# Kernel tuning notes

Measured on AMD Instinct MI355X. Metric: run time of the kernel, lower is better.

The kernel has to match this reference:

```python
import jax, jax.numpy as jnp
import numpy as np

H = 50  # hidden size hard-coded in the module

def _lstm_cell(x, h, c, Wih, Whh, bih, bhh):
    # torch.nn.LSTMCell: gates ordered i, f, g, o
    g = x @ Wih.T + bih + h @ Whh.T + bhh  # [B, 4H]
    i, f, gg, o = jnp.split(g, 4, axis=-1)
    c2 = jax.nn.sigmoid(f) * c + jax.nn.sigmoid(i) * jnp.tanh(gg)
    h2 = jax.nn.sigmoid(o) * jnp.tanh(c2)
    return h2, c2

def setup_inputs() -> dict:
    key = jax.random.key(0)
    ks = jax.random.split(key, 10)
    B, T = 2048, 1024
    s1 = 1.0 / np.sqrt(H)
    u = lambda k, shp: jax.random.uniform(k, shp, jnp.float32, -s1, s1)
    return {
        "x": jax.random.normal(ks[0], (B, T), jnp.float32),
        "W_ih1": u(ks[1], (4 * H, 1)),
        "W_hh1": u(ks[2], (4 * H, H)),
        "b_ih1": u(ks[3], (4 * H,)),
        "b_hh1": u(ks[4], (4 * H,)),
        "W_ih2": u(ks[5], (4 * H, H)),
        "W_hh2": u(ks[6], (4 * H, H)),
        "b_ih2": u(ks[7], (4 * H,)),
        "b_hh2": u(ks[8], (4 * H,)),
        "W_lin": u(ks[9], (1, H)),
        "b_lin": jnp.zeros((1,), jnp.float32),
    }

def reference(x, W_ih1, W_hh1, b_ih1, b_hh1, W_ih2, W_hh2, b_ih2, b_hh2, W_lin, b_lin):
    # future=0 path; dropout is identity in eval mode.
    B = x.shape[0]
    xT = x.T[:, :, None]  # [T, B, 1]
    z = jnp.zeros((B, H), x.dtype)

    def step(carry, xt):
        h1, c1, h2, c2 = carry
        h1, c1 = _lstm_cell(xt, h1, c1, W_ih1, W_hh1, b_ih1, b_hh1)
        h2, c2 = _lstm_cell(h1, h2, c2, W_ih2, W_hh2, b_ih2, b_hh2)
        return (h1, c1, h2, c2), None

    (h1, c1, h2, c2), _ = jax.lax.scan(step, (z, z, z, z), xT)
    # outputs[:, -1] == linear(h_t2) at the final timestep
    out = h2 @ W_lin.T + b_lin  # [B, 1]
    return out[:, 0]
```

## Files before the change

### kernel.cpp

```cpp
#include <hip/hip_runtime.h>


#define TT 1024
#define HH 50
#define NB 8
#define NT 832
#define NTILE 13
#define VSZ 2112

typedef _Float16 f16x8 __attribute__((ext_vector_type(8)));
typedef unsigned short ushort8 __attribute__((ext_vector_type(8)));
typedef float f32x4 __attribute__((ext_vector_type(4)));

#define NLOG2E  -1.4426950408889634f
#define N2LOG2E -2.8853900817779268f

__device__ __forceinline__ float fast_rcp(float x) { return __builtin_amdgcn_rcpf(x); }
__device__ __forceinline__ float exp2f_hw(float x) { return __builtin_amdgcn_exp2f(x); }
__device__ __forceinline__ unsigned short f16bits(float f) {
    _Float16 h = (_Float16)f;
    return __builtin_bit_cast(unsigned short, h);
}
__device__ __forceinline__ float f16tof(unsigned short b) {
    return (float)__builtin_bit_cast(_Float16, b);
}
__device__ __forceinline__ float dpp_merge(float a, float b) {
    return __int_as_float(__builtin_amdgcn_update_dpp(
        __float_as_int(a), __float_as_int(b), 0x118, 0xF, 0xC, false));
}

__device__ __forceinline__ int vidx(int k, int n) {
    return ((k >> 3) << 7) + n * 8 + (k & 7);
}

__global__ __launch_bounds__(NT) void lstm_kernel(
    const float* __restrict__ x,
    const float* __restrict__ W_ih1, const float* __restrict__ W_hh1,
    const float* __restrict__ b_ih1, const float* __restrict__ b_hh1,
    const float* __restrict__ W_ih2, const float* __restrict__ W_hh2,
    const float* __restrict__ b_ih2, const float* __restrict__ b_hh2,
    const float* __restrict__ W_lin, const float* __restrict__ b_lin,
    float* __restrict__ out)
{
    __shared__ float xs[TT * NB];
    __shared__ __attribute__((aligned(16))) unsigned short v[2][VSZ];

    const int tid  = threadIdx.x;
    const int w    = tid >> 6;
    const int L    = tid & 63;
    const int quad = L >> 4;
    const int n15  = L & 15;
    const int b0g  = blockIdx.x * NB;

    const int  m     = w;
    const int  u     = m * 4 + quad;
    const bool low   = (n15 < NB);
    const bool updOK = (u < HH);
    const bool ldB   = low;
    const bool xw    = (w == 12) && (L >= 32) && (L < 32 + NB);
    const int  xb    = L - 32;
    const int hslot = updOK ? (low ? vidx(1 + u, n15) : vidx(51 + u, n15 - NB))
                            : (2048 + L);

    for (int i = tid; i < 2 * VSZ; i += NT) ((unsigned short*)v)[i] = 0;
    for (int i = tid; i < NB * TT; i += NT) {
        int b = i >> 10, t = i & 1023;
        xs[t * NB + b] = x[(size_t)b0g * TT + i];
    }

    f16x8 a1[2], a2[4];
    f32x4 bias1 = {0.f, 0.f, 0.f, 0.f}, bias2 = {0.f, 0.f, 0.f, 0.f};
    float c = 0.f;

    {
        const int arow = m * 16 + n15;
        const bool av = (arow < 200);
        const int r = av ? ((arow & 3) * 50 + (arow >> 2)) : 0;
        const float sc = ((arow & 3) == 2) ? N2LOG2E : NLOG2E;
        #pragma unroll
        for (int kt = 0; kt < 2; ++kt) {
            ushort8 th;
            #pragma unroll
            for (int j = 0; j < 8; ++j) {
                int k = kt * 32 + quad * 8 + j;
                float wv = 0.f;
                if (av) { if (k == 0) wv = W_ih1[r]; else if (k <= 50) wv = W_hh1[r * 50 + k - 1]; }
                th[j] = f16bits(wv * sc);
            }
            a1[kt] = __builtin_bit_cast(f16x8, th);
        }
        #pragma unroll
        for (int kt = 0; kt < 4; ++kt) {
            ushort8 th;
            #pragma unroll
            for (int j = 0; j < 8; ++j) {
                int k = kt * 32 + quad * 8 + j;
                float wv = 0.f;
                if (av) {
                    if (k >= 1 && k <= 50) wv = W_ih2[r * 50 + k - 1];
                    else if (k >= 51 && k <= 100) wv = W_hh2[r * 50 + k - 51];
                }
                th[j] = f16bits(wv * sc);
            }
            a2[kt] = __builtin_bit_cast(f16x8, th);
        }
        #pragma unroll
        for (int reg = 0; reg < 4; ++reg) {
            int crow = m * 16 + quad * 4 + reg;
            if (crow < 200) {
                int rr = (crow & 3) * 50 + (crow >> 2);
                float s2 = ((crow & 3) == 2) ? N2LOG2E : NLOG2E;
                bias1[reg] = s2 * (b_ih1[rr] + b_hh1[rr]);
                bias2[reg] = s2 * (b_ih2[rr] + b_hh2[rr]);
            }
        }
    }

    __syncthreads();
    if (tid < NB) v[0][vidx(0, tid)] = f16bits(xs[0 * NB + tid]);
    __syncthreads();

    f16x8 bfr[4];
    #pragma unroll
    for (int kt = 0; kt < 4; ++kt)
        bfr[kt] = __builtin_bit_cast(f16x8, ushort8{0,0,0,0,0,0,0,0});

    auto body = [&](int t, const unsigned short* vr, unsigned short* vw,
                    bool doL1, bool doL2, bool masked) {
        if (ldB) {
            #pragma unroll
            for (int kt = 0; kt < 4; ++kt)
                bfr[kt] = ((const f16x8*)vr)[kt * 64 + L];
        }
        f32x4 aM1 = bias1, aM2 = bias2;
        if (doL1) {
            #pragma unroll
            for (int kt = 0; kt < 2; ++kt)
                aM1 = __builtin_amdgcn_mfma_f32_16x16x32_f16(a1[kt], bfr[kt], aM1, 0, 0, 0);
        }
        if (doL2) {
            #pragma unroll
            for (int kt = 0; kt < 4; ++kt)
                aM2 = __builtin_amdgcn_mfma_f32_16x16x32_f16(a2[kt], bfr[kt], aM2, 0, 0, 0);
        }
        f32x4 g;
        #pragma unroll
        for (int r = 0; r < 4; ++r) g[r] = dpp_merge(aM1[r], aM2[r]);

        if (!masked || (updOK && low)) {
            float ei = exp2f_hw(g[0]);
            float ef = exp2f_hw(g[1]);
            float eg = exp2f_hw(g[2]);
            float eo = exp2f_hw(g[3]);
            float p  = (1.0f + ei) * (1.0f + eg);
            float q  = (1.0f - eg) * (1.0f + ef);
            float cn = fmaf(c, p, q) * fast_rcp(p * (1.0f + ef));
            c = cn;
            float ecn = exp2f_hw(cn * N2LOG2E);
            float h = (1.0f - ecn) * fast_rcp((1.0f + eo) * (1.0f + ecn));
            vw[hslot] = f16bits(h);
        }
        if (xw && t + 1 < TT) vw[vidx(0, xb)] = f16bits(xs[(t + 1) * NB + xb]);
        __syncthreads();
    };

    body(0, v[0], v[1], true, false, true);
    body(1, v[1], v[0], true, true, false);
    for (int t = 2; t < TT; t += 2) {
        body(t,     v[0], v[1], true, true, false);
        body(t + 1, v[1], v[0], true, true, false);
    }
    body(TT, v[0], v[1], false, true, false);

    if (tid < NB) {
        float s = b_lin[0];
        #pragma unroll
        for (int uu = 0; uu < HH; ++uu)
            s += W_lin[uu] * f16tof(v[1][vidx(51 + uu, tid)]);
        out[b0g + tid] = s;
    }
}

extern "C" void kernel_launch(void* const* d_in, const int* in_sizes, int n_in,
                              void* d_out, int out_size, void* d_ws, size_t ws_size,
                              hipStream_t stream) {
    const float* x     = (const float*)d_in[0];
    const float* W_ih1 = (const float*)d_in[1];
    const float* W_hh1 = (const float*)d_in[2];
    const float* b_ih1 = (const float*)d_in[3];
    const float* b_hh1 = (const float*)d_in[4];
    const float* W_ih2 = (const float*)d_in[5];
    const float* W_hh2 = (const float*)d_in[6];
    const float* b_ih2 = (const float*)d_in[7];
    const float* b_hh2 = (const float*)d_in[8];
    const float* W_lin = (const float*)d_in[9];
    const float* b_lin = (const float*)d_in[10];
    float* out = (float*)d_out;

    const int Btot = in_sizes[0] / TT;
    const int nblocks = Btot / NB;

    lstm_kernel<<<nblocks, NT, 0, stream>>>(
        x, W_ih1, W_hh1, b_ih1, b_hh1, W_ih2, W_hh2, b_ih2, b_hh2,
        W_lin, b_lin, out);
}
```

Measured before the change: 535.5 us.

## Assign two MFMA row tiles per wave to halve the waves per block

Each wave now handles two of the 13 gate-row tiles instead of one, so the block shrinks from 13 waves to 7. Every wave keeps two sets of weight fragments, biases and cell states, and runs two cell updates per timestep. The aim is to lower the cost of the per-timestep __syncthreads barrier and the redundant B-fragment loads by having fewer waves. In exchange each wave does twice the serial MFMA and transcendental work on the critical path and needs more registers.

```diff
diff --git a/kernel.cpp b/kernel.cpp
--- a/kernel.cpp
+++ b/kernel.cpp
@@ -4,7 +4,7 @@
 #define TT 1024
 #define HH 50
 #define NB 8
-#define NT 832
+#define NT 448
 #define NTILE 13
 #define VSZ 2112
 
@@ -52,15 +52,21 @@
     const int n15  = L & 15;
     const int b0g  = blockIdx.x * NB;
 
-    const int  m     = w;
-    const int  u     = m * 4 + quad;
+    const int  m0    = 2 * w;
+    const int  m1    = 2 * w + 1;
+    const bool hasT1 = (m1 < NTILE);
+    const int  u0    = m0 * 4 + quad;
+    const int  u1    = m1 * 4 + quad;
     const bool low   = (n15 < NB);
-    const bool updOK = (u < HH);
+    const bool upd0  = (u0 < HH);
+    const bool upd1  = (u1 < HH);
     const bool ldB   = low;
-    const bool xw    = (w == 12) && (L >= 32) && (L < 32 + NB);
+    const bool xw    = (w == 6) && (L >= 32) && (L < 32 + NB);
     const int  xb    = L - 32;
-    const int hslot = updOK ? (low ? vidx(1 + u, n15) : vidx(51 + u, n15 - NB))
-                            : (2048 + L);
+    const int hs0 = upd0 ? (low ? vidx(1 + u0, n15) : vidx(51 + u0, n15 - NB))
+                         : (2048 + L);
+    const int hs1 = upd1 ? (low ? vidx(1 + u1, n15) : vidx(51 + u1, n15 - NB))
+                         : (2048 + L);
 
     for (int i = tid; i < 2 * VSZ; i += NT) ((unsigned short*)v)[i] = 0;
     for (int i = tid; i < NB * TT; i += NT) {
@@ -68,11 +74,11 @@
         xs[t * NB + b] = x[(size_t)b0g * TT + i];
     }
 
-    f16x8 a1[2], a2[4];
-    f32x4 bias1 = {0.f, 0.f, 0.f, 0.f}, bias2 = {0.f, 0.f, 0.f, 0.f};
-    float c = 0.f;
-
-    {
+    f16x8 a1_0[2], a2_0[4], a1_1[2], a2_1[4];
+    f32x4 b1_0, b2_0, b1_1, b2_1;
+    float cA = 0.f, cB = 0.f;
+
+    auto initA = [&](int m, f16x8* a1t, f16x8* a2t, f32x4& b1t, f32x4& b2t) {
         const int arow = m * 16 + n15;
         const bool av = (arow < 200);
         const int r = av ? ((arow & 3) * 50 + (arow >> 2)) : 0;
@@ -87,7 +93,7 @@
                 if (av) { if (k == 0) wv = W_ih1[r]; else if (k <= 50) wv = W_hh1[r * 50 + k - 1]; }
                 th[j] = f16bits(wv * sc);
             }
-            a1[kt] = __builtin_bit_cast(f16x8, th);
+            a1t[kt] = __builtin_bit_cast(f16x8, th);
         }
         #pragma unroll
         for (int kt = 0; kt < 4; ++kt) {
@@ -102,19 +108,23 @@
                 }
                 th[j] = f16bits(wv * sc);
             }
-            a2[kt] = __builtin_bit_cast(f16x8, th);
+            a2t[kt] = __builtin_bit_cast(f16x8, th);
         }
         #pragma unroll
         for (int reg = 0; reg < 4; ++reg) {
+            float bv1 = 0.f, bv2 = 0.f;
             int crow = m * 16 + quad * 4 + reg;
             if (crow < 200) {
                 int rr = (crow & 3) * 50 + (crow >> 2);
                 float s2 = ((crow & 3) == 2) ? N2LOG2E : NLOG2E;
-                bias1[reg] = s2 * (b_ih1[rr] + b_hh1[rr]);
-                bias2[reg] = s2 * (b_ih2[rr] + b_hh2[rr]);
-            }
-        }
-    }
+                bv1 = s2 * (b_ih1[rr] + b_hh1[rr]);
+                bv2 = s2 * (b_ih2[rr] + b_hh2[rr]);
+            }
+            b1t[reg] = bv1; b2t[reg] = bv2;
+        }
+    };
+    initA(m0, a1_0, a2_0, b1_0, b2_0);
+    initA(m1, a1_1, a2_1, b1_1, b2_1);
 
     __syncthreads();
     if (tid < NB) v[0][vidx(0, tid)] = f16bits(xs[0 * NB + tid]);
@@ -125,6 +135,20 @@
     for (int kt = 0; kt < 4; ++kt)
         bfr[kt] = __builtin_bit_cast(f16x8, ushort8{0,0,0,0,0,0,0,0});
 
+    auto cell = [&](float& c, const f32x4& g, int hs, unsigned short* vw) {
+        float ei = exp2f_hw(g[0]);
+        float ef = exp2f_hw(g[1]);
+        float eg = exp2f_hw(g[2]);
+        float eo = exp2f_hw(g[3]);
+        float p  = (1.0f + ei) * (1.0f + eg);
+        float q  = (1.0f - eg) * (1.0f + ef);
+        float cn = fmaf(c, p, q) * fast_rcp(p * (1.0f + ef));
+        c = cn;
+        float ecn = exp2f_hw(cn * N2LOG2E);
+        float h = (1.0f - ecn) * fast_rcp((1.0f + eo) * (1.0f + ecn));
+        vw[hs] = f16bits(h);
+    };
+
     auto body = [&](int t, const unsigned short* vr, unsigned short* vw,
                     bool doL1, bool doL2, bool masked) {
         if (ldB) {
@@ -132,33 +156,39 @@
             for (int kt = 0; kt < 4; ++kt)
                 bfr[kt] = ((const f16x8*)vr)[kt * 64 + L];
         }
-        f32x4 aM1 = bias1, aM2 = bias2;
+        f32x4 aM1a = b1_0, aM2a = b2_0;
+        f32x4 aM1b = b1_1, aM2b = b2_1;
         if (doL1) {
             #pragma unroll
             for (int kt = 0; kt < 2; ++kt)
-                aM1 = __builtin_amdgcn_mfma_f32_16x16x32_f16(a1[kt], bfr[kt], aM1, 0, 0, 0);
+                aM1a = __builtin_amdgcn_mfma_f32_16x16x32_f16(a1_0[kt], bfr[kt], aM1a, 0, 0, 0);
+            if (hasT1) {
+                #pragma unroll
+                for (int kt = 0; kt < 2; ++kt)
+                    aM1b = __builtin_amdgcn_mfma_f32_16x16x32_f16(a1_1[kt], bfr[kt], aM1b, 0, 0, 0);
+            }
         }
         if (doL2) {
             #pragma unroll
             for (int kt = 0; kt < 4; ++kt)
-                aM2 = __builtin_amdgcn_mfma_f32_16x16x32_f16(a2[kt], bfr[kt], aM2, 0, 0, 0);
-        }
-        f32x4 g;
-        #pragma unroll
-        for (int r = 0; r < 4; ++r) g[r] = dpp_merge(aM1[r], aM2[r]);
-
-        if (!masked || (updOK && low)) {
-            float ei = exp2f_hw(g[0]);
-            float ef = exp2f_hw(g[1]);
-            float eg = exp2f_hw(g[2]);
-            float eo = exp2f_hw(g[3]);
-            float p  = (1.0f + ei) * (1.0f + eg);
-            float q  = (1.0f - eg) * (1.0f + ef);
-            float cn = fmaf(c, p, q) * fast_rcp(p * (1.0f + ef));
-            c = cn;
-            float ecn = exp2f_hw(cn * N2LOG2E);
-            float h = (1.0f - ecn) * fast_rcp((1.0f + eo) * (1.0f + ecn));
-            vw[hslot] = f16bits(h);
+                aM2a = __builtin_amdgcn_mfma_f32_16x16x32_f16(a2_0[kt], bfr[kt], aM2a, 0, 0, 0);
+            if (hasT1) {
+                #pragma unroll
+                for (int kt = 0; kt < 4; ++kt)
+                    aM2b = __builtin_amdgcn_mfma_f32_16x16x32_f16(a2_1[kt], bfr[kt], aM2b, 0, 0, 0);
+            }
+        }
+        {
+            f32x4 g;
+            #pragma unroll
+            for (int r = 0; r < 4; ++r) g[r] = dpp_merge(aM1a[r], aM2a[r]);
+            if (!masked || (upd0 && low)) cell(cA, g, hs0, vw);
+        }
+        if (hasT1) {
+            f32x4 g;
+            #pragma unroll
+            for (int r = 0; r < 4; ++r) g[r] = dpp_merge(aM1b[r], aM2b[r]);
+            if (!masked || (upd1 && low)) cell(cB, g, hs1, vw);
         }
         if (xw && t + 1 < TT) vw[vidx(0, xb)] = f16bits(xs[(t + 1) * NB + xb]);
         __syncthreads();
@@ -193,8 +223,8 @@
     const float* W_hh2 = (const float*)d_in[6];
     const float* b_ih2 = (const float*)d_in[7];
     const float* b_hh2 = (const float*)d_in[8];
+    const float* b_lin = (const float*)d_in[10];
     const float* W_lin = (const float*)d_in[9];
-    const float* b_lin = (const float*)d_in[10];
     float* out = (float*)d_out;
 
     const int Btot = in_sizes[0] / TT;
```

Measured after the change: 589.9 us. 10.1% more time.
